# Kernel tuning notes

Hardware: AMD Instinct MI355X
Metric: run time of the kernel (lower is better)

## Reference

```python
import jax, jax.numpy as jnp
import numpy as np

B, S, D, H = 2, 2048, 1024, 16
DK = D // H


def setup_inputs() -> dict:
    key = jax.random.key(0)
    ks = jax.random.split(key, 8)
    query = jax.random.normal(ks[0], (B, S, D), dtype=jnp.float32)
    key_t = jax.random.normal(ks[1], (B, S, D), dtype=jnp.float32)
    value = jax.random.normal(ks[2], (B, S, D), dtype=jnp.float32)
    # causal mask (1 = attend, 0 = masked), broadcast over batch and heads
    mask = jnp.tril(jnp.ones((S, S), dtype=jnp.int32))[None, None, :, :]
    scale = 1.0 / np.sqrt(D)
    w_q = jax.random.normal(ks[3], (D, D), dtype=jnp.float32) * scale
    w_k = jax.random.normal(ks[4], (D, D), dtype=jnp.float32) * scale
    w_v = jax.random.normal(ks[5], (D, D), dtype=jnp.float32) * scale
    w_o = jax.random.normal(ks[6], (D, D), dtype=jnp.float32) * scale
    b_o = jnp.zeros((D,), dtype=jnp.float32)
    return {"query": query, "key": key_t, "value": value, "mask": mask,
            "w_q": w_q, "w_k": w_k, "w_v": w_v, "w_o": w_o, "b_o": b_o}


def reference(query, key, value, mask, w_q, w_k, w_v, w_o, b_o):
    # projections: nn.Linear applies x @ W.T; weights here stored as [out, in]
    def proj(x, w):  # [B,S,D] -> [B,H,S,DK]
        y = jnp.einsum('bsd,ed->bse', x, w)
        return y.reshape(B, S, H, DK).transpose(0, 2, 1, 3)

    Q = proj(query, w_q)
    K = proj(key, w_k)
    V = proj(value, w_v)

    scores = jnp.einsum('bhqd,bhkd->bhqk', Q, K) / jnp.sqrt(jnp.float32(DK))
    scores = jnp.where(mask == 0, jnp.float32(-1e9), scores)
    attention_weights = jax.nn.softmax(scores, axis=-1)  # dropout p=0 (eval)
    context = jnp.einsum('bhqk,bhkd->bhqd', attention_weights, V)
    context = context.transpose(0, 2, 1, 3).reshape(B, S, D)
    output = jnp.einsum('bsd,ed->bse', context, w_o) + b_o
    return output, attention_weights
```

## Files before the change

### kernel.cpp

```cpp
#include <hip/hip_runtime.h>
#include <hip/hip_bf16.h>
#include <math.h>

#define B_  2
#define S_  2048
#define D_  1024
#define H_  16
#define DK_ 64

typedef __attribute__((ext_vector_type(8))) short bf16x8;
typedef __attribute__((ext_vector_type(4))) float f32x4;
typedef __attribute__((ext_vector_type(8))) unsigned short u16x8;
typedef __attribute__((ext_vector_type(4))) unsigned short u16x4;

#define MFMA16(a, b, c) __builtin_amdgcn_mfma_f32_16x16x32_bf16((a), (b), (c), 0, 0, 0)

__device__ __forceinline__ unsigned short f2bf(float f) {
    union { float f; unsigned u; } v; v.f = f;
    unsigned r = v.u + 0x7fffu + ((v.u >> 16) & 1u);
    return (unsigned short)(r >> 16);
}
__device__ __forceinline__ float bf2f(unsigned short u) {
    return __uint_as_float(((unsigned)u) << 16);
}

__global__ __launch_bounds__(256) void cvt_all(
        const float* __restrict__ q, const float* __restrict__ k, const float* __restrict__ v,
        const float* __restrict__ wq, const float* __restrict__ wk,
        const float* __restrict__ wv, const float* __restrict__ wo,
        unsigned short* __restrict__ xq, unsigned short* __restrict__ xk,
        unsigned short* __restrict__ xv, unsigned short* __restrict__ wqb,
        unsigned short* __restrict__ wkb, unsigned short* __restrict__ wvb,
        unsigned short* __restrict__ wob) {
    int i = blockIdx.x * 256 + threadIdx.x;
    const float* src; unsigned short* dst; int off;
    if      (i < 1048576) { src = q;  dst = xq;  off = 0; }
    else if (i < 2097152) { src = k;  dst = xk;  off = 1048576; }
    else if (i < 3145728) { src = v;  dst = xv;  off = 2097152; }
    else if (i < 3407872) { src = wq; dst = wqb; off = 3145728; }
    else if (i < 3670016) { src = wk; dst = wkb; off = 3407872; }
    else if (i < 3932160) { src = wv; dst = wvb; off = 3670016; }
    else                  { src = wo; dst = wob; off = 3932160; }
    i -= off;
    f32x4 f = __builtin_nontemporal_load(reinterpret_cast<const f32x4*>(src) + i);
    ushort4 o;
    o.x = f2bf(f[0]); o.y = f2bf(f[1]); o.z = f2bf(f[2]); o.w = f2bf(f[3]);
    reinterpret_cast<ushort4*>(dst)[i] = o;
}

__device__ __forceinline__ void gemm_bt_body(char* myep, int blk,
        const unsigned short* __restrict__ A, const unsigned short* __restrict__ W,
        void* __restrict__ out, const float* __restrict__ bias, int mode, float scale) {
    const int lane = threadIdx.x & 63;
    const int row  = lane & 15, quad = lane >> 4;
    const int w    = threadIdx.x >> 6;
    const int wid  = blk * 4 + w;
    const int m0   = (wid & 127) * 32;
    const int n0   = (wid >> 7) * 64;
    f32x4 acc[2][4] = {};
    const unsigned short* Ap = A + (m0 + row) * D_ + quad * 8;
    const unsigned short* Wp = W + (n0 + row) * D_ + quad * 8;
    for (int k0 = 0; k0 < D_; k0 += 32) {
        bf16x8 a0 = *(const bf16x8*)(Ap + k0);
        bf16x8 a1 = *(const bf16x8*)(Ap + 16 * D_ + k0);
        bf16x8 w0 = *(const bf16x8*)(Wp + k0);
        bf16x8 w1 = *(const bf16x8*)(Wp + 16 * D_ + k0);
        bf16x8 w2 = *(const bf16x8*)(Wp + 32 * D_ + k0);
        bf16x8 w3 = *(const bf16x8*)(Wp + 48 * D_ + k0);
        acc[0][0] = MFMA16(a0, w0, acc[0][0]);
        acc[0][1] = MFMA16(a0, w1, acc[0][1]);
        acc[0][2] = MFMA16(a0, w2, acc[0][2]);
        acc[0][3] = MFMA16(a0, w3, acc[0][3]);
        acc[1][0] = MFMA16(a1, w0, acc[1][0]);
        acc[1][1] = MFMA16(a1, w1, acc[1][1]);
        acc[1][2] = MFMA16(a1, w2, acc[1][2]);
        acc[1][3] = MFMA16(a1, w3, acc[1][3]);
    }
    const int b = m0 >> 11;
    const int h = n0 >> 6;
    if (mode == 0) {
        unsigned short* lt = (unsigned short*)myep;
#pragma unroll
        for (int mi = 0; mi < 2; mi++)
#pragma unroll
            for (int t = 0; t < 4; t++)
#pragma unroll
                for (int r = 0; r < 4; r++)
                    lt[(mi * 16 + quad * 4 + r) * 72 + t * 16 + row] = f2bf(acc[mi][t][r] * scale);
        __builtin_amdgcn_sched_barrier(0);
        unsigned short* Qout = (unsigned short*)out;
#pragma unroll
        for (int pass = 0; pass < 4; pass++) {
            int rr = pass * 8 + (lane >> 3);
            int cc = (lane & 7) * 8;
            u16x8 val = *(const u16x8*)(lt + rr * 72 + cc);
            int s = (m0 + rr) & (S_ - 1);
            *(u16x8*)(&Qout[(((size_t)(b * H_ + h)) * S_ + s) * DK_ + cc]) = val;
        }
    } else if (mode == 1) {
        unsigned short* lt = (unsigned short*)myep;
#pragma unroll
        for (int mi = 0; mi < 2; mi++)
#pragma unroll
            for (int t = 0; t < 4; t++)
#pragma unroll
                for (int r = 0; r < 4; r++)
                    lt[(t * 16 + row) * 40 + mi * 16 + quad * 4 + r] = f2bf(acc[mi][t][r]);
        __builtin_amdgcn_sched_barrier(0);
        unsigned short* Vout = (unsigned short*)out;
#pragma unroll
        for (int pass = 0; pass < 8; pass++) {
            int dk = pass * 8 + (lane >> 3);
            int so = (lane & 7) * 4;
            u16x4 val = *(const u16x4*)(lt + dk * 40 + so);
            *(u16x4*)(&Vout[(((size_t)(b * H_ + h)) * DK_ + dk) * S_ + (m0 & (S_ - 1)) + so]) = val;
        }
    } else {
        float* lt32 = (float*)myep;
        float bs[4];
#pragma unroll
        for (int t = 0; t < 4; t++) bs[t] = bias[n0 + t * 16 + row];
#pragma unroll
        for (int mi = 0; mi < 2; mi++)
#pragma unroll
            for (int t = 0; t < 4; t++)
#pragma unroll
                for (int r = 0; r < 4; r++)
                    lt32[(mi * 16 + quad * 4 + r) * 72 + t * 16 + row] = acc[mi][t][r] + bs[t];
        __builtin_amdgcn_sched_barrier(0);
        float* outF = (float*)out;
#pragma unroll
        for (int pass = 0; pass < 8; pass++) {
            int rr = pass * 4 + (lane >> 4);
            int cc = (lane & 15) * 4;
            f32x4 val = *(const f32x4*)(lt32 + rr * 72 + cc);
            __builtin_nontemporal_store(val, (f32x4*)(&outF[(size_t)(m0 + rr) * D_ + n0 + cc]));
        }
    }
}

__global__ __launch_bounds__(256) void gemm_qkv(
        const unsigned short* __restrict__ xq, const unsigned short* __restrict__ xk,
        const unsigned short* __restrict__ xv, const unsigned short* __restrict__ wqb,
        const unsigned short* __restrict__ wkb, const unsigned short* __restrict__ wvb,
        unsigned short* __restrict__ Qb, unsigned short* __restrict__ Kb,
        unsigned short* __restrict__ Vt) {
    __shared__ char eplds[4 * 5120];
    char* myep = eplds + (threadIdx.x >> 6) * 5120;
    const int which = blockIdx.x >> 9;
    const int blk   = blockIdx.x & 511;
    if (which == 0)      gemm_bt_body(myep, blk, xq, wqb, Qb, nullptr, 0, 0.125f);
    else if (which == 1) gemm_bt_body(myep, blk, xk, wkb, Kb, nullptr, 0, 1.0f);
    else                 gemm_bt_body(myep, blk, xv, wvb, Vt, nullptr, 1, 1.0f);
}

__global__ __launch_bounds__(256) void gemm_out(
        const unsigned short* __restrict__ A, const unsigned short* __restrict__ W,
        float* __restrict__ out, const float* __restrict__ bias) {
    __shared__ char eplds[4 * 9216];
    gemm_bt_body(eplds + (threadIdx.x >> 6) * 9216, blockIdx.x, A, W, out, bias, 2, 1.0f);
}

__global__ __launch_bounds__(256) void attn_kernel(const unsigned short* __restrict__ Qb,
                                                   const unsigned short* __restrict__ Kb,
                                                   const unsigned short* __restrict__ Vt,
                                                   float* __restrict__ Pbase,
                                                   unsigned short* __restrict__ ctx) {
    __shared__ unsigned short plds[4][16 * 40];
    __shared__ float olds[4][16 * 64];
    __shared__ float llds[4][16];
    const int w    = threadIdx.x >> 6;
    const int lane = threadIdx.x & 63;
    const int row  = lane & 15, quad = lane >> 4;
    const int tile = 127 - (int)(blockIdx.x >> 5);
    const int bh   = blockIdx.x & 31;
    const int q0   = tile * 16;
    const int b    = bh >> 4, h = bh & 15;
    const unsigned short* Qh = Qb + (size_t)bh * S_ * DK_;
    const unsigned short* Kh = Kb + (size_t)bh * S_ * DK_;
    const unsigned short* Vh = Vt + (size_t)bh * DK_ * S_;
    float* P = Pbase + (size_t)bh * S_ * S_;

    bf16x8 aq0 = *(const bf16x8*)(Qh + (q0 + row) * DK_ + quad * 8);
    bf16x8 aq1 = *(const bf16x8*)(Qh + (q0 + row) * DK_ + 32 + quad * 8);

    const int nks   = (q0 + 47) >> 5;
    const int nfull = (q0 + 1) >> 5;

    float l_l[4] = {0.f, 0.f, 0.f, 0.f};
    for (int ks = w; ks < nks; ks += 4) {
        const int c0k = ks * 32;
        const bool diag = (ks >= nfull);
#pragma unroll
        for (int half = 0; half < 2; half++) {
            const int c = c0k + half * 16;
            const unsigned short* kp = Kh + (c + row) * DK_ + quad * 8;
            bf16x8 k0 = *(const bf16x8*)kp;
            bf16x8 k1 = *(const bf16x8*)(kp + 32);
            f32x4 sa = {};
            sa = MFMA16(aq0, k0, sa);
            sa = MFMA16(aq1, k1, sa);
#pragma unroll
            for (int r = 0; r < 4; r++) {
                float p = __expf(sa[r]);
                if (diag) p = ((c + row) <= (q0 + quad * 4 + r)) ? p : 0.f;
                l_l[r] += p;
            }
        }
    }
#pragma unroll
    for (int r = 0; r < 4; r++) {
#pragma unroll
        for (int off = 1; off < 16; off <<= 1)
            l_l[r] += __shfl_xor(l_l[r], off, 16);
        if (row == 0) llds[w][quad * 4 + r] = l_l[r];
    }
    __syncthreads();
    float invL[4];
#pragma unroll
    for (int r = 0; r < 4; r++)
        invL[r] = 1.0f / (llds[0][quad * 4 + r] + llds[1][quad * 4 + r] +
                          llds[2][quad * 4 + r] + llds[3][quad * 4 + r]);

    f32x4 o[4] = {};
    unsigned short* myld = plds[w];
    for (int ks = w; ks < nks; ks += 4) {
        const int c0k = ks * 32;
        const bool diag = (ks >= nfull);
#pragma unroll
        for (int half = 0; half < 2; half++) {
            const int c = c0k + half * 16;
            const unsigned short* kp = Kh + (c + row) * DK_ + quad * 8;
            bf16x8 k0 = *(const bf16x8*)kp;
            bf16x8 k1 = *(const bf16x8*)(kp + 32);
            f32x4 sa = {};
            sa = MFMA16(aq0, k0, sa);
            sa = MFMA16(aq1, k1, sa);
#pragma unroll
            for (int r = 0; r < 4; r++) {
                float p = __expf(sa[r]) * invL[r];
                if (diag) p = ((c + row) <= (q0 + quad * 4 + r)) ? p : 0.f;
                myld[(quad * 4 + r) * 40 + half * 16 + row] = f2bf(p);
            }
        }
        __builtin_amdgcn_sched_barrier(0);
#pragma unroll
        for (int g = 0; g < 2; g++) {
            int rr = g * 8 + (lane >> 3);
            int cg = (lane & 7) * 4;
            u16x4 pb = *(const u16x4*)(myld + rr * 40 + cg);
            f32x4 pv;
            pv[0] = bf2f((unsigned short)pb[0]);
            pv[1] = bf2f((unsigned short)pb[1]);
            pv[2] = bf2f((unsigned short)pb[2]);
            pv[3] = bf2f((unsigned short)pb[3]);
            __builtin_nontemporal_store(pv, (f32x4*)(&P[(size_t)(q0 + rr) * S_ + c0k + cg]));
        }
        bf16x8 pf = *(const bf16x8*)(myld + row * 40 + quad * 8);
#pragma unroll
        for (int t4 = 0; t4 < 4; t4++) {
            bf16x8 vv = *(const bf16x8*)(Vh + (t4 * 16 + row) * S_ + c0k + quad * 8);
            o[t4] = MFMA16(pf, vv, o[t4]);
        }
        __builtin_amdgcn_sched_barrier(0);
    }

    float* myo = olds[w];
#pragma unroll
    for (int t4 = 0; t4 < 4; t4++)
#pragma unroll
        for (int r = 0; r < 4; r++)
            myo[(quad * 4 + r) * 64 + t4 * 16 + row] = o[t4][r];
    __syncthreads();
    {
        int i  = threadIdx.x;
        int rr = i >> 4, c4 = (i & 15) * 4;
        u16x4 cv;
#pragma unroll
        for (int j = 0; j < 4; j++) {
            float s = olds[0][rr * 64 + c4 + j] + olds[1][rr * 64 + c4 + j] +
                      olds[2][rr * 64 + c4 + j] + olds[3][rr * 64 + c4 + j];
            cv[j] = (short)f2bf(s);
        }
        *(u16x4*)(&ctx[((size_t)(b * S_) + q0 + rr) * D_ + h * DK_ + c4]) = cv;
    }

    const int cb = nks * 32;
    if (cb < S_) {
        const int nq = (S_ - cb) >> 2;
        const f32x4 z = {0.f, 0.f, 0.f, 0.f};
        for (int i = threadIdx.x; i < 16 * nq; i += 256) {
            int rr = i / nq, cc = i - rr * nq;
            __builtin_nontemporal_store(z,
                reinterpret_cast<f32x4*>(&P[(size_t)(q0 + rr) * S_ + cb + cc * 4]));
        }
    }
}

extern "C" void kernel_launch(void* const* d_in, const int* in_sizes, int n_in,
                              void* d_out, int out_size, void* d_ws, size_t ws_size,
                              hipStream_t stream) {
    const float* q  = (const float*)d_in[0];
    const float* k  = (const float*)d_in[1];
    const float* v  = (const float*)d_in[2];
    const float* wq = (const float*)d_in[4];
    const float* wk = (const float*)d_in[5];
    const float* wv = (const float*)d_in[6];
    const float* wo = (const float*)d_in[7];
    const float* bo = (const float*)d_in[8];

    unsigned short* ws  = (unsigned short*)d_ws;
    unsigned short* xq  = ws;
    unsigned short* xk  = ws + 4194304;
    unsigned short* xv  = ws + 8388608;
    unsigned short* wqb = ws + 12582912;
    unsigned short* wkb = wqb + 1048576;
    unsigned short* wvb = wkb + 1048576;
    unsigned short* wob = wvb + 1048576;
    unsigned short* Qb  = ws + 16777216;
    unsigned short* Kb  = Qb + 4194304;
    unsigned short* Vt  = Kb + 4194304;
    unsigned short* ctx = Vt + 4194304;
    float* outp  = (float*)d_out;
    float* Pbase = outp + 4194304;

    cvt_all<<<16384, 256, 0, stream>>>(q, k, v, wq, wk, wv, wo,
                                       xq, xk, xv, wqb, wkb, wvb, wob);

    gemm_qkv<<<1536, 256, 0, stream>>>(xq, xk, xv, wqb, wkb, wvb, Qb, Kb, Vt);

    attn_kernel<<<4096, 256, 0, stream>>>(Qb, Kb, Vt, Pbase, ctx);

    gemm_out<<<512, 256, 0, stream>>>(ctx, wob, outp, bo);
}
```

Before: 884.8 us.

## Enlarge GEMM per-wave tiles to 64x64 and simplify P zero-fill loop

Each wave in the projection GEMMs now computes a 64x64 output tile instead of 32x64, with blocks covering 128x128 so more MFMAs are issued per A/W fragment load. Grid sizes are halved, epilogue LDS staging grows to match, and the output GEMM writes its tile in two halves. The masked-region zero fill of the attention-probability matrix now walks rows with contiguous column strides instead of using an integer divide per element. The trade-off is more accumulator registers, which may lower occupancy, and fewer blocks in flight.

```diff
diff --git a/kernel.cpp b/kernel.cpp
--- a/kernel.cpp
+++ b/kernel.cpp
@@ -54,15 +54,18 @@
     const int lane = threadIdx.x & 63;
     const int row  = lane & 15, quad = lane >> 4;
     const int w    = threadIdx.x >> 6;
-    const int wid  = blk * 4 + w;
-    const int m0   = (wid & 127) * 32;
-    const int n0   = (wid >> 7) * 64;
-    f32x4 acc[2][4] = {};
+    const int bmi  = blk & 31;
+    const int bni  = blk >> 5;
+    const int m0   = bmi * 128 + (w >> 1) * 64;
+    const int n0   = bni * 128 + (w & 1) * 64;
+    f32x4 acc[4][4] = {};
     const unsigned short* Ap = A + (m0 + row) * D_ + quad * 8;
     const unsigned short* Wp = W + (n0 + row) * D_ + quad * 8;
     for (int k0 = 0; k0 < D_; k0 += 32) {
         bf16x8 a0 = *(const bf16x8*)(Ap + k0);
         bf16x8 a1 = *(const bf16x8*)(Ap + 16 * D_ + k0);
+        bf16x8 a2 = *(const bf16x8*)(Ap + 32 * D_ + k0);
+        bf16x8 a3 = *(const bf16x8*)(Ap + 48 * D_ + k0);
         bf16x8 w0 = *(const bf16x8*)(Wp + k0);
         bf16x8 w1 = *(const bf16x8*)(Wp + 16 * D_ + k0);
         bf16x8 w2 = *(const bf16x8*)(Wp + 32 * D_ + k0);
@@ -75,13 +78,21 @@
         acc[1][1] = MFMA16(a1, w1, acc[1][1]);
         acc[1][2] = MFMA16(a1, w2, acc[1][2]);
         acc[1][3] = MFMA16(a1, w3, acc[1][3]);
+        acc[2][0] = MFMA16(a2, w0, acc[2][0]);
+        acc[2][1] = MFMA16(a2, w1, acc[2][1]);
+        acc[2][2] = MFMA16(a2, w2, acc[2][2]);
+        acc[2][3] = MFMA16(a2, w3, acc[2][3]);
+        acc[3][0] = MFMA16(a3, w0, acc[3][0]);
+        acc[3][1] = MFMA16(a3, w1, acc[3][1]);
+        acc[3][2] = MFMA16(a3, w2, acc[3][2]);
+        acc[3][3] = MFMA16(a3, w3, acc[3][3]);
     }
     const int b = m0 >> 11;
     const int h = n0 >> 6;
     if (mode == 0) {
         unsigned short* lt = (unsigned short*)myep;
 #pragma unroll
-        for (int mi = 0; mi < 2; mi++)
+        for (int mi = 0; mi < 4; mi++)
 #pragma unroll
             for (int t = 0; t < 4; t++)
 #pragma unroll
@@ -90,7 +101,7 @@
         __builtin_amdgcn_sched_barrier(0);
         unsigned short* Qout = (unsigned short*)out;
 #pragma unroll
-        for (int pass = 0; pass < 4; pass++) {
+        for (int pass = 0; pass < 8; pass++) {
             int rr = pass * 8 + (lane >> 3);
             int cc = (lane & 7) * 8;
             u16x8 val = *(const u16x8*)(lt + rr * 72 + cc);
@@ -100,41 +111,47 @@
     } else if (mode == 1) {
         unsigned short* lt = (unsigned short*)myep;
 #pragma unroll
-        for (int mi = 0; mi < 2; mi++)
+        for (int mi = 0; mi < 4; mi++)
 #pragma unroll
             for (int t = 0; t < 4; t++)
 #pragma unroll
                 for (int r = 0; r < 4; r++)
-                    lt[(t * 16 + row) * 40 + mi * 16 + quad * 4 + r] = f2bf(acc[mi][t][r]);
+                    lt[(t * 16 + row) * 72 + mi * 16 + quad * 4 + r] = f2bf(acc[mi][t][r]);
         __builtin_amdgcn_sched_barrier(0);
         unsigned short* Vout = (unsigned short*)out;
 #pragma unroll
         for (int pass = 0; pass < 8; pass++) {
             int dk = pass * 8 + (lane >> 3);
-            int so = (lane & 7) * 4;
-            u16x4 val = *(const u16x4*)(lt + dk * 40 + so);
-            *(u16x4*)(&Vout[(((size_t)(b * H_ + h)) * DK_ + dk) * S_ + (m0 & (S_ - 1)) + so]) = val;
+            int so = (lane & 7) * 8;
+            u16x8 val = *(const u16x8*)(lt + dk * 72 + so);
+            *(u16x8*)(&Vout[(((size_t)(b * H_ + h)) * DK_ + dk) * S_ + (m0 & (S_ - 1)) + so]) = val;
         }
     } else {
         float* lt32 = (float*)myep;
         float bs[4];
 #pragma unroll
         for (int t = 0; t < 4; t++) bs[t] = bias[n0 + t * 16 + row];
-#pragma unroll
-        for (int mi = 0; mi < 2; mi++)
-#pragma unroll
-            for (int t = 0; t < 4; t++)
-#pragma unroll
-                for (int r = 0; r < 4; r++)
-                    lt32[(mi * 16 + quad * 4 + r) * 72 + t * 16 + row] = acc[mi][t][r] + bs[t];
-        __builtin_amdgcn_sched_barrier(0);
         float* outF = (float*)out;
 #pragma unroll
-        for (int pass = 0; pass < 8; pass++) {
-            int rr = pass * 4 + (lane >> 4);
-            int cc = (lane & 15) * 4;
-            f32x4 val = *(const f32x4*)(lt32 + rr * 72 + cc);
-            __builtin_nontemporal_store(val, (f32x4*)(&outF[(size_t)(m0 + rr) * D_ + n0 + cc]));
+        for (int mh = 0; mh < 2; mh++) {
+#pragma unroll
+            for (int mi2 = 0; mi2 < 2; mi2++)
+#pragma unroll
+                for (int t = 0; t < 4; t++)
+#pragma unroll
+                    for (int r = 0; r < 4; r++)
+                        lt32[(mi2 * 16 + quad * 4 + r) * 72 + t * 16 + row] =
+                            acc[mh * 2 + mi2][t][r] + bs[t];
+            __builtin_amdgcn_sched_barrier(0);
+#pragma unroll
+            for (int pass = 0; pass < 8; pass++) {
+                int rr = pass * 4 + (lane >> 4);
+                int cc = (lane & 15) * 4;
+                f32x4 val = *(const f32x4*)(lt32 + rr * 72 + cc);
+                __builtin_nontemporal_store(val,
+                    (f32x4*)(&outF[(size_t)(m0 + mh * 32 + rr) * D_ + n0 + cc]));
+            }
+            __builtin_amdgcn_sched_barrier(0);
         }
     }
 }
@@ -145,10 +162,10 @@
         const unsigned short* __restrict__ wkb, const unsigned short* __restrict__ wvb,
         unsigned short* __restrict__ Qb, unsigned short* __restrict__ Kb,
         unsigned short* __restrict__ Vt) {
-    __shared__ char eplds[4 * 5120];
-    char* myep = eplds + (threadIdx.x >> 6) * 5120;
-    const int which = blockIdx.x >> 9;
-    const int blk   = blockIdx.x & 511;
+    __shared__ char eplds[4 * 9216];
+    char* myep = eplds + (threadIdx.x >> 6) * 9216;
+    const int which = blockIdx.x >> 8;
+    const int blk   = blockIdx.x & 255;
     if (which == 0)      gemm_bt_body(myep, blk, xq, wqb, Qb, nullptr, 0, 0.125f);
     else if (which == 1) gemm_bt_body(myep, blk, xk, wkb, Kb, nullptr, 0, 1.0f);
     else                 gemm_bt_body(myep, blk, xv, wvb, Vt, nullptr, 1, 1.0f);
@@ -287,12 +304,12 @@
 
     const int cb = nks * 32;
     if (cb < S_) {
-        const int nq = (S_ - cb) >> 2;
         const f32x4 z = {0.f, 0.f, 0.f, 0.f};
-        for (int i = threadIdx.x; i < 16 * nq; i += 256) {
-            int rr = i / nq, cc = i - rr * nq;
-            __builtin_nontemporal_store(z,
-                reinterpret_cast<f32x4*>(&P[(size_t)(q0 + rr) * S_ + cb + cc * 4]));
+#pragma unroll 1
+        for (int rr = 0; rr < 16; rr++) {
+            float* Pr = &P[(size_t)(q0 + rr) * S_];
+            for (int cc = cb + threadIdx.x * 4; cc < S_; cc += 1024)
+                __builtin_nontemporal_store(z, reinterpret_cast<f32x4*>(Pr + cc));
         }
     }
 }
@@ -327,9 +344,9 @@
     cvt_all<<<16384, 256, 0, stream>>>(q, k, v, wq, wk, wv, wo,
                                        xq, xk, xv, wqb, wkb, wvb, wob);
 
-    gemm_qkv<<<1536, 256, 0, stream>>>(xq, xk, xv, wqb, wkb, wvb, Qb, Kb, Vt);
+    gemm_qkv<<<768, 256, 0, stream>>>(xq, xk, xv, wqb, wkb, wvb, Qb, Kb, Vt);
 
     attn_kernel<<<4096, 256, 0, stream>>>(Qb, Kb, Vt, Pbase, ctx);
 
-    gemm_out<<<512, 256, 0, stream>>>(ctx, wob, outp, bo);
-}
+    gemm_out<<<256, 256, 0, stream>>>(ctx, wob, outp, bo);
+}
```

After: 858.4 us. 1.03x faster.
